# Performance work log

Hardware: AMD Instinct MI355X
Metric: run time of the kernel (lower is better)

Reference implementation:

```python
import jax, jax.numpy as jnp
import numpy as np

# Module hyper-parameters (match init_kwargs)
WIN = 64        # windowSize -> N
REC = 128       # receptiveSize -> M
H = 8           # numHeads
D = 32          # headDim
DIM = 256       # dim
MAXD = WIN + (REC - WIN) // 2  # maxDisparity = 96

# Static relative position index table, shape (N, M), values in [0, 2*MAXD)
_coords_x = np.arange(WIN)[:, None]
_coords_x_ = (np.arange(REC) - (REC - WIN) // 2)[None, :]
REL_IDX = jnp.asarray(_coords_x - _coords_x_ + MAXD, dtype=jnp.int32)


def setup_inputs() -> dict:
    key = jax.random.key(0)
    ks = jax.random.split(key, 12)
    B, nW = 4, 256
    B_ = B * nW
    x = jax.random.normal(ks[0], (B_, WIN, DIM), jnp.float32)
    x_ = jax.random.normal(ks[1], (B_, REC, DIM), jnp.float32)
    mask_left = jax.random.randint(ks[2], (2, WIN, REC), 0, 2, jnp.int32)
    mask_right = jax.random.randint(ks[3], (2, WIN, REC), 0, 2, jnp.int32)
    s = 0.02
    q_w = jax.random.normal(ks[4], (DIM, H * D), jnp.float32) * s
    q_b = jnp.zeros((H * D,), jnp.float32)
    kv_w = jax.random.normal(ks[5], (DIM, 2 * H * D), jnp.float32) * s
    kv_b = jnp.zeros((2 * H * D,), jnp.float32)
    proj_w = jax.random.normal(ks[6], (H * D, DIM), jnp.float32) * s
    proj_b = jnp.zeros((DIM,), jnp.float32)
    bias_table = jax.random.normal(ks[7], (2 * MAXD, H), jnp.float32) * s
    return dict(x=x, x_=x_, mask_left=mask_left, mask_right=mask_right, nW=nW,
                q_w=q_w, q_b=q_b, kv_w=kv_w, kv_b=kv_b,
                proj_w=proj_w, proj_b=proj_b, bias_table=bias_table)


def reference(x, x_, mask_left, mask_right, nW, q_w, q_b, kv_w, kv_b, proj_w, proj_b, bias_table):
    B_, N, C = x.shape
    M = x_.shape[1]
    B = B_ // nW
    scale = D ** -0.5

    q = (x @ q_w + q_b).reshape(B_, N, H, D).transpose(0, 2, 1, 3)   # b h n d
    kv = x_ @ kv_w + kv_b
    k, v = jnp.split(kv, 2, axis=-1)
    k = k.reshape(B_, M, H, D).transpose(0, 2, 1, 3)                 # b h m d
    v = v.reshape(B_, M, H, D).transpose(0, 2, 1, 3)                 # b h m d

    attn = jnp.einsum('bhnd,bhmd->bhnm', q, k) * scale
    # gathered relative position bias: (N, M, H) -> (H, N, M)
    bias = bias_table[REL_IDX].transpose(2, 0, 1)
    attn = attn + bias[None]

    mask_value = -jnp.finfo(attn.dtype).max
    attn = attn.reshape(B, nW, H, N, M)
    mc = min(mask_left.shape[0], nW)  # static python int
    ml = (mask_left[:mc] == 1)[None, :, None]        # (1, mc, 1, N, M)
    attn = attn.at[:, :mc].set(jnp.where(ml, mask_value, attn[:, :mc]))
    mr = (mask_right[mask_right.shape[0] - mc:] == 1)[None, :, None]
    attn = attn.at[:, nW - mc:].set(jnp.where(mr, mask_value, attn[:, nW - mc:]))
    attn = attn.reshape(B_, H, N, M)

    attn = jax.nn.softmax(attn, axis=-1)
    out = jnp.einsum('bhnm,bhmd->bhnd', attn, v)
    out = out.transpose(0, 2, 1, 3).reshape(B_, N, H * D)
    out = out @ proj_w + proj_b
    return out
```

## Files before the change

### kernel.cpp

```cpp
#include <hip/hip_runtime.h>
#include <float.h>


typedef __attribute__((ext_vector_type(8))) short bf16x8;
typedef __attribute__((ext_vector_type(4))) float f32x4;

static __device__ __forceinline__ unsigned int f2bf(float f) {
    unsigned int u = __float_as_uint(f);
    return (u + 0x7FFFu + ((u >> 16) & 1u)) >> 16;
}
static __device__ __forceinline__ unsigned int pack2(float lo, float hi) {
    return f2bf(lo) | (f2bf(hi) << 16);
}

__device__ unsigned short g_Wt[262144];

__global__ __launch_bounds__(256) void prep_wt(
    const float* __restrict__ q_w, const float* __restrict__ kv_w, const float* __restrict__ proj_w)
{
    const int gid = blockIdx.x * 256 + threadIdx.x;
    int rel, ncs; const float* src;
    if (gid < 65536)       { rel = gid;          src = q_w;    ncs = 256; }
    else if (gid < 196608) { rel = gid - 65536;  src = kv_w;   ncs = 512; }
    else                   { rel = gid - 196608; src = proj_w; ncs = 256; }
    const int tl = rel >> 11, i = rel & 2047;
    const int ct = tl >> 3,  ks = tl & 7;
    const int col = i >> 5,  si = i & 31;
    const int kl = ((2 * si) ^ ((col & 3) << 4)) >> 1;
    g_Wt[gid] = (unsigned short)f2bf(src[(ks * 32 + kl) * ncs + ct * 64 + col]);
}

template<int NC, int WT_OFF, bool ABF16, bool F32OUT>
__global__ __launch_bounds__(256) void gemm_t(
    const void* __restrict__ Ain, const float* __restrict__ bias, void* __restrict__ Cout)
{
    constexpr int NCT = NC / 64;
    __shared__ __align__(16) unsigned short As[2][4096];
    __shared__ __align__(16) unsigned short Ws[2][2048];

    const int nbx = 8 * NCT;
    const int g = blockIdx.x / nbx, r = blockIdx.x % nbx;
    const int bn = r >> 3, bm = g * 8 + (r & 7);
    const size_t r0 = (size_t)bm * 128;
    const int c0 = bn * 64;

    const int t = threadIdx.x;
    const int wave = t >> 6, lane = t & 63;
    const int lr = lane & 15, hi = lane >> 4;
    const int rw = (wave >> 1) * 64, cw = (wave & 1) * 32;

    const int arow = t >> 1, aseg = t & 1;
    const int aswz = (arow & 3) << 4;
    const int ao0 = (aseg * 32) ^ aswz, ao1 = (aseg * 32 + 16) ^ aswz;

    f32x4 acc[4][2];
    #pragma unroll
    for (int i = 0; i < 4; ++i)
        #pragma unroll
        for (int j = 0; j < 2; ++j) acc[i][j] = (f32x4){0.f, 0.f, 0.f, 0.f};

    float4 ra0, ra1, ra2, ra3;
    uint4  rb0, rb1;
    uint4  rwv;

#define GLOAD(S)                                                                           \
    {                                                                                      \
        rwv = *(const uint4*)(g_Wt + WT_OFF + ((size_t)(bn * 8 + (S)) << 11) + t * 8);     \
        if (ABF16) {                                                                       \
            const unsigned short* asrc = (const unsigned short*)Ain + (r0 + arow) * 256 + (S) * 32 + aseg * 16; \
            rb0 = *(const uint4*)asrc; rb1 = *(const uint4*)(asrc + 8);                    \
        } else {                                                                           \
            const float* asrc = (const float*)Ain + (r0 + arow) * 256 + (S) * 32 + aseg * 16; \
            ra0 = *(const float4*)asrc;       ra1 = *(const float4*)(asrc + 4);            \
            ra2 = *(const float4*)(asrc + 8); ra3 = *(const float4*)(asrc + 12);           \
        }                                                                                  \
    }

#define SWRITE(B)                                                                          \
    {                                                                                      \
        uint4 u0, u1;                                                                      \
        if (ABF16) { u0 = rb0; u1 = rb1; }                                                 \
        else {                                                                             \
            u0 = make_uint4(pack2(ra0.x, ra0.y), pack2(ra0.z, ra0.w),                      \
                            pack2(ra1.x, ra1.y), pack2(ra1.z, ra1.w));                     \
            u1 = make_uint4(pack2(ra2.x, ra2.y), pack2(ra2.z, ra2.w),                      \
                            pack2(ra3.x, ra3.y), pack2(ra3.z, ra3.w));                     \
        }                                                                                  \
        char* ad = (char*)As[B] + arow * 64;                                               \
        *(uint4*)(ad + ao0) = u0; *(uint4*)(ad + ao1) = u1;                                \
        *(uint4*)((char*)Ws[B] + t * 16) = rwv;                                            \
    }

#define COMPUTE(B)                                                                         \
    {                                                                                      \
        const char* Ab = (const char*)As[B];                                               \
        const char* Wb = (const char*)Ws[B];                                               \
        const int ko = (16 * hi) ^ ((lr & 3) << 4);                                        \
        bf16x8 af0 = *(const bf16x8*)(Ab + (rw +      lr) * 64 + ko);                      \
        bf16x8 af1 = *(const bf16x8*)(Ab + (rw + 16 + lr) * 64 + ko);                      \
        bf16x8 af2 = *(const bf16x8*)(Ab + (rw + 32 + lr) * 64 + ko);                      \
        bf16x8 af3 = *(const bf16x8*)(Ab + (rw + 48 + lr) * 64 + ko);                      \
        bf16x8 bg0 = *(const bf16x8*)(Wb + (cw +      lr) * 64 + ko);                      \
        bf16x8 bg1 = *(const bf16x8*)(Wb + (cw + 16 + lr) * 64 + ko);                      \
        acc[0][0] = __builtin_amdgcn_mfma_f32_16x16x32_bf16(af0, bg0, acc[0][0], 0, 0, 0); \
        acc[0][1] = __builtin_amdgcn_mfma_f32_16x16x32_bf16(af0, bg1, acc[0][1], 0, 0, 0); \
        acc[1][0] = __builtin_amdgcn_mfma_f32_16x16x32_bf16(af1, bg0, acc[1][0], 0, 0, 0); \
        acc[1][1] = __builtin_amdgcn_mfma_f32_16x16x32_bf16(af1, bg1, acc[1][1], 0, 0, 0); \
        acc[2][0] = __builtin_amdgcn_mfma_f32_16x16x32_bf16(af2, bg0, acc[2][0], 0, 0, 0); \
        acc[2][1] = __builtin_amdgcn_mfma_f32_16x16x32_bf16(af2, bg1, acc[2][1], 0, 0, 0); \
        acc[3][0] = __builtin_amdgcn_mfma_f32_16x16x32_bf16(af3, bg0, acc[3][0], 0, 0, 0); \
        acc[3][1] = __builtin_amdgcn_mfma_f32_16x16x32_bf16(af3, bg1, acc[3][1], 0, 0, 0); \
    }

    GLOAD(0); SWRITE(0); __syncthreads();

    #pragma unroll 8
    for (int s = 0; s < 8; ++s) {
        if (s < 7) GLOAD(s + 1);
        COMPUTE(s & 1);
        if (s < 7) {
            SWRITE((s + 1) & 1);
            __syncthreads();
        }
    }

#undef GLOAD
#undef SWRITE
#undef COMPUTE

    #pragma unroll
    for (int i = 0; i < 4; ++i) {
        #pragma unroll
        for (int bj = 0; bj < 2; ++bj) {
            const int col = c0 + cw + bj * 16 + lr;
            const float bb = bias[col];
            #pragma unroll
            for (int q = 0; q < 4; ++q) {
                const size_t row = r0 + rw + i * 16 + 4 * hi + q;
                const float val = acc[i][bj][q] + bb;
                if (F32OUT) ((float*)Cout)[row * NC + col] = val;
                else        ((unsigned short*)Cout)[row * NC + col] = (unsigned short)f2bf(val);
            }
        }
    }
}

__global__ __launch_bounds__(256) void attn_fused(
    const unsigned short* __restrict__ qbf, const unsigned short* __restrict__ kvbf,
    const float* __restrict__ bias_table, const int* __restrict__ mask_left,
    const int* __restrict__ mask_right, unsigned short* __restrict__ aout)
{
    __shared__ __align__(16) unsigned short Qn[64 * 32];
    __shared__ __align__(16) unsigned short Kn[128 * 32];
    __shared__ __align__(16) unsigned short Vt[32 * 128];
    __shared__ __align__(16) unsigned short Pn[64 * 128];
    __shared__ float ballT[8 * 192];

    const int w = blockIdx.x;
    const int t = threadIdx.x;
    const int wave = t >> 6, lane = t & 63;
    const int lr = lane & 15, hi = lane >> 4;
    const int n0w = wave * 16;

    for (int i = t; i < 1536; i += 256) {
        const int hh = i / 192, r = i - hh * 192;
        ballT[i] = bias_table[r * 8 + hh];
    }

    const int wi = w & 255;
    const int* mbase = nullptr;
    if (wi < 2) mbase = mask_left + wi * (64 * 128);
    else if (wi >= 254) mbase = mask_right + (wi - 254) * (64 * 128);

    const float scale = 0.17677669529663687f;

    for (int h = 0; h < 8; ++h) {
        __syncthreads();
        {
            const int n = t >> 2, dq = t & 3;
            const uint4 v = *(const uint4*)(qbf + ((size_t)(w * 64 + n)) * 256 + h * 32 + dq * 8);
            *(uint4*)((char*)Qn + n * 64 + dq * 16) = v;
        }
        #pragma unroll
        for (int i = 0; i < 2; ++i) {
            const int m = (t >> 2) + 64 * i, dq = t & 3;
            const uint4 v = *(const uint4*)(kvbf + ((size_t)(w * 128 + m)) * 512 + h * 32 + dq * 8);
            *(uint4*)((char*)Kn + m * 64 + dq * 16) = v;
        }
        #pragma unroll
        for (int i = 0; i < 2; ++i) {
            const int db = (t >> 7) * 2 + i, m = t & 127;
            const uint4 v = *(const uint4*)(kvbf + ((size_t)(w * 128 + m)) * 512 + 256 + h * 32 + db * 8);
            const unsigned short* vs = (const unsigned short*)&v;
            #pragma unroll
            for (int e = 0; e < 8; ++e) {
                const int d = db * 8 + e;
                *(unsigned short*)((char*)Vt + d * 256 + ((2 * m) ^ ((d & 7) << 4))) = vs[e];
            }
        }
        __syncthreads();

        const bf16x8 qa = *(const bf16x8*)((char*)Qn + (n0w + lr) * 64 + 16 * hi);
        f32x4 sacc[8];
        #pragma unroll
        for (int mj = 0; mj < 8; ++mj) {
            sacc[mj] = (f32x4){0.f, 0.f, 0.f, 0.f};
            const bf16x8 kb = *(const bf16x8*)((char*)Kn + (mj * 16 + lr) * 64 + 16 * hi);
            sacc[mj] = __builtin_amdgcn_mfma_f32_16x16x32_bf16(qa, kb, sacc[mj], 0, 0, 0);
        }

        const float* bh = ballT + h * 192;
        #pragma unroll
        for (int mj = 0; mj < 8; ++mj) {
            const int m = 16 * mj + lr;
            #pragma unroll
            for (int q = 0; q < 4; ++q) {
                const int n = n0w + 4 * hi + q;
                sacc[mj][q] = fmaf(sacc[mj][q], scale, bh[n - m + 128]);
            }
        }
        if (mbase) {
            #pragma unroll
            for (int mj = 0; mj < 8; ++mj) {
                const int m = 16 * mj + lr;
                #pragma unroll
                for (int q = 0; q < 4; ++q) {
                    const int n = n0w + 4 * hi + q;
                    if (mbase[n * 128 + m] == 1) sacc[mj][q] = -FLT_MAX;
                }
            }
        }

        float inv[4];
        #pragma unroll
        for (int q = 0; q < 4; ++q) {
            float mx = sacc[0][q];
            #pragma unroll
            for (int mj = 1; mj < 8; ++mj) mx = fmaxf(mx, sacc[mj][q]);
            mx = fmaxf(mx, __shfl_xor(mx, 1));
            mx = fmaxf(mx, __shfl_xor(mx, 2));
            mx = fmaxf(mx, __shfl_xor(mx, 4));
            mx = fmaxf(mx, __shfl_xor(mx, 8));
            float sm = 0.f;
            #pragma unroll
            for (int mj = 0; mj < 8; ++mj) {
                sacc[mj][q] = __expf(sacc[mj][q] - mx);
                sm += sacc[mj][q];
            }
            sm += __shfl_xor(sm, 1);
            sm += __shfl_xor(sm, 2);
            sm += __shfl_xor(sm, 4);
            sm += __shfl_xor(sm, 8);
            inv[q] = 1.0f / sm;
        }

        #pragma unroll
        for (int mj = 0; mj < 8; ++mj) {
            #pragma unroll
            for (int q = 0; q < 4; ++q) {
                const float pv = sacc[mj][q];
                const float po = __shfl_xor(pv, 1);
                if (!(lane & 1)) {
                    const int n = n0w + 4 * hi + q;
                    const int m = 16 * mj + lr;
                    const unsigned int u = f2bf(pv) | (f2bf(po) << 16);
                    *(unsigned int*)((char*)Pn + n * 256 + ((2 * m) ^ ((n & 7) << 4))) = u;
                }
            }
        }

        f32x4 oacc[2];
        oacc[0] = (f32x4){0.f, 0.f, 0.f, 0.f};
        oacc[1] = (f32x4){0.f, 0.f, 0.f, 0.f};
        const int nA = n0w + lr;
        const int swzA = (nA & 7) << 4;
        #pragma unroll
        for (int kk = 0; kk < 4; ++kk) {
            const bf16x8 pa = *(const bf16x8*)((char*)Pn + nA * 256 + ((64 * kk + 16 * hi) ^ swzA));
            #pragma unroll
            for (int j = 0; j < 2; ++j) {
                const int d = j * 16 + lr;
                const bf16x8 vb = *(const bf16x8*)((char*)Vt + d * 256 + ((64 * kk + 16 * hi) ^ ((d & 7) << 4)));
                oacc[j] = __builtin_amdgcn_mfma_f32_16x16x32_bf16(pa, vb, oacc[j], 0, 0, 0);
            }
        }
        #pragma unroll
        for (int j = 0; j < 2; ++j) {
            #pragma unroll
            for (int q = 0; q < 4; ++q) {
                const int n = n0w + 4 * hi + q;
                aout[((size_t)(w * 64 + n)) * 256 + h * 32 + j * 16 + lr] =
                    (unsigned short)f2bf(oacc[j][q] * inv[q]);
            }
        }
    }
}

extern "C" void kernel_launch(void* const* d_in, const int* in_sizes, int n_in,
                              void* d_out, int out_size, void* d_ws, size_t ws_size,
                              hipStream_t stream)
{
    const float* x      = (const float*)d_in[0];
    const float* x_     = (const float*)d_in[1];
    const int*   mask_l = (const int*)d_in[2];
    const int*   mask_r = (const int*)d_in[3];
    const float* q_w    = (const float*)d_in[5];
    const float* q_b    = (const float*)d_in[6];
    const float* kv_w   = (const float*)d_in[7];
    const float* kv_b   = (const float*)d_in[8];
    const float* proj_w = (const float*)d_in[9];
    const float* proj_b = (const float*)d_in[10];
    const float* bias_t = (const float*)d_in[11];

    unsigned short* qbf  = (unsigned short*)d_ws;
    unsigned short* kvbf = qbf + (size_t)65536 * 256;
    float* out = (float*)d_out;

    prep_wt<<<1024, 256, 0, stream>>>(q_w, kv_w, proj_w);
    gemm_t<256, 0,      false, false><<<2048, 256, 0, stream>>>(x,  q_b,  qbf);
    gemm_t<512, 65536,  false, false><<<8192, 256, 0, stream>>>(x_, kv_b, kvbf);
    attn_fused<<<1024, 256, 0, stream>>>(qbf, kvbf, bias_t, mask_l, mask_r, qbf);
    gemm_t<256, 196608, true,  true ><<<2048, 256, 0, stream>>>(qbf, proj_b, out);
}
```

Measured before the change: 302.2 us.

## Fuse KV projection GEMM into attention kernel, computing K/V per head in LDS

Removes the separate KV projection GEMM and its bf16 global intermediate. Each attention block now loads its 128x256 slice of x_ into LDS as bf16 and computes K and V per head with MFMA, staging the weight slice in LDS. This saves the global write and reread of the KV tensor and one kernel launch. In exchange, LDS use per block grows a lot (about 64KB for XL plus 32KB for weights), which lowers occupancy, and the weights are reloaded from global memory for each head in each block.

Measured after the change: 319.9 us. 5.9% more time.

```diff
diff --git a/kernel.cpp b/kernel.cpp
--- a/kernel.cpp
+++ b/kernel.cpp
@@ -145,26 +145,52 @@
     }
 }
 
-__global__ __launch_bounds__(256) void attn_fused(
-    const unsigned short* __restrict__ qbf, const unsigned short* __restrict__ kvbf,
-    const float* __restrict__ bias_table, const int* __restrict__ mask_left,
-    const int* __restrict__ mask_right, unsigned short* __restrict__ aout)
+__global__ __launch_bounds__(256) void attn_kv(
+    const unsigned short* __restrict__ qbf, const float* __restrict__ x_,
+    const float* __restrict__ kv_bias, const float* __restrict__ bias_table,
+    const int* __restrict__ mask_left, const int* __restrict__ mask_right,
+    unsigned short* __restrict__ aout)
 {
-    __shared__ __align__(16) unsigned short Qn[64 * 32];
+    __shared__ __align__(16) unsigned short XL[128 * 256];
+    __shared__ __align__(16) unsigned short W2s[8 * 2048];
     __shared__ __align__(16) unsigned short Kn[128 * 32];
     __shared__ __align__(16) unsigned short Vt[32 * 128];
     __shared__ __align__(16) unsigned short Pn[64 * 128];
+    __shared__ __align__(16) unsigned short Qn[64 * 32];
     __shared__ float ballT[8 * 192];
+    __shared__ float kvb[512];
 
     const int w = blockIdx.x;
     const int t = threadIdx.x;
     const int wave = t >> 6, lane = t & 63;
     const int lr = lane & 15, hi = lane >> 4;
     const int n0w = wave * 16;
+    const int rw4 = wave * 32;
 
     for (int i = t; i < 1536; i += 256) {
-        const int hh = i / 192, r = i - hh * 192;
-        ballT[i] = bias_table[r * 8 + hh];
+        const int hh = i / 192, rr = i - hh * 192;
+        ballT[i] = bias_table[rr * 8 + hh];
+    }
+    kvb[t] = kv_bias[t];
+    kvb[t + 256] = kv_bias[t + 256];
+
+    {
+        const int row = t >> 1, half = t & 1;
+        const float* src = x_ + ((size_t)(w * 128 + row)) * 256 + half * 128;
+        char* dst = (char*)XL + row * 512;
+        const int swz = (row & 7) << 4;
+        #pragma unroll 2
+        for (int u = 0; u < 8; ++u) {
+            const float4 a = *(const float4*)(src + u * 16);
+            const float4 b = *(const float4*)(src + u * 16 + 4);
+            const float4 c = *(const float4*)(src + u * 16 + 8);
+            const float4 d = *(const float4*)(src + u * 16 + 12);
+            const int base = half * 256 + u * 32;
+            *(uint4*)(dst + (base ^ swz)) =
+                make_uint4(pack2(a.x, a.y), pack2(a.z, a.w), pack2(b.x, b.y), pack2(b.z, b.w));
+            *(uint4*)(dst + ((base + 16) ^ swz)) =
+                make_uint4(pack2(c.x, c.y), pack2(c.z, c.w), pack2(d.x, d.y), pack2(d.z, d.w));
+        }
     }
 
     const int wi = w & 255;
@@ -176,26 +202,75 @@
 
     for (int h = 0; h < 8; ++h) {
         __syncthreads();
+
+        {
+            const uint4* wsrc = (const uint4*)(g_Wt + 65536);
+            uint4* wdst = (uint4*)W2s;
+            const int ctK = h >> 1, half = h & 1;
+            #pragma unroll
+            for (int u = 0; u < 8; ++u) {
+                const int idx = t + u * 256;
+                const int ks = idx >> 8;
+                const int kvh = (idx >> 7) & 1;
+                const int off = idx & 127;
+                const int ct = kvh ? (4 + ctK) : ctK;
+                wdst[idx] = wsrc[(ct * 8 + ks) * 256 + half * 128 + off];
+            }
+        }
         {
             const int n = t >> 2, dq = t & 3;
             const uint4 v = *(const uint4*)(qbf + ((size_t)(w * 64 + n)) * 256 + h * 32 + dq * 8);
             *(uint4*)((char*)Qn + n * 64 + dq * 16) = v;
         }
+        __syncthreads();
+
+        f32x4 kacc[2][4];
+        #pragma unroll
+        for (int i = 0; i < 2; ++i)
+            #pragma unroll
+            for (int j = 0; j < 4; ++j) kacc[i][j] = (f32x4){0.f, 0.f, 0.f, 0.f};
+
+        {
+            const int swzX = (lr & 7) << 4;
+            const int ko2  = (16 * hi) ^ ((lr & 3) << 4);
+            #pragma unroll
+            for (int ks = 0; ks < 8; ++ks) {
+                const int koX = (ks * 64 + 16 * hi) ^ swzX;
+                const bf16x8 af0 = *(const bf16x8*)((char*)XL + (rw4 +      lr) * 512 + koX);
+                const bf16x8 af1 = *(const bf16x8*)((char*)XL + (rw4 + 16 + lr) * 512 + koX);
+                const char* wb = (const char*)W2s + ks * 4096;
+                #pragma unroll
+                for (int j = 0; j < 4; ++j) {
+                    const bf16x8 bfr = *(const bf16x8*)(wb + (j * 16 + lr) * 64 + ko2);
+                    kacc[0][j] = __builtin_amdgcn_mfma_f32_16x16x32_bf16(af0, bfr, kacc[0][j], 0, 0, 0);
+                    kacc[1][j] = __builtin_amdgcn_mfma_f32_16x16x32_bf16(af1, bfr, kacc[1][j], 0, 0, 0);
+                }
+            }
+        }
         #pragma unroll
         for (int i = 0; i < 2; ++i) {
-            const int m = (t >> 2) + 64 * i, dq = t & 3;
-            const uint4 v = *(const uint4*)(kvbf + ((size_t)(w * 128 + m)) * 512 + h * 32 + dq * 8);
-            *(uint4*)((char*)Kn + m * 64 + dq * 16) = v;
-        }
-        #pragma unroll
-        for (int i = 0; i < 2; ++i) {
-            const int db = (t >> 7) * 2 + i, m = t & 127;
-            const uint4 v = *(const uint4*)(kvbf + ((size_t)(w * 128 + m)) * 512 + 256 + h * 32 + db * 8);
-            const unsigned short* vs = (const unsigned short*)&v;
-            #pragma unroll
-            for (int e = 0; e < 8; ++e) {
-                const int d = db * 8 + e;
-                *(unsigned short*)((char*)Vt + d * 256 + ((2 * m) ^ ((d & 7) << 4))) = vs[e];
+            #pragma unroll
+            for (int j = 0; j < 2; ++j) {
+                const int d = j * 16 + lr;
+                const float bb = kvb[h * 32 + d];
+                #pragma unroll
+                for (int q = 0; q < 4; ++q) {
+                    const float kv_ = kacc[i][j][q] + bb;
+                    const float po = __shfl_xor(kv_, 1);
+                    if (!(lane & 1)) {
+                        const int m = rw4 + i * 16 + 4 * hi + q;
+                        *(unsigned int*)((char*)Kn + m * 64 + 2 * d) = f2bf(kv_) | (f2bf(po) << 16);
+                    }
+                }
+            }
+            #pragma unroll
+            for (int j = 2; j < 4; ++j) {
+                const int d = (j - 2) * 16 + lr;
+                const float bb = kvb[256 + h * 32 + d];
+                const int m0 = rw4 + i * 16 + 4 * hi;
+                const unsigned int lo = pack2(kacc[i][j][0] + bb, kacc[i][j][1] + bb);
+                const unsigned int h2 = pack2(kacc[i][j][2] + bb, kacc[i][j][3] + bb);
+                *(uint2*)((char*)Vt + d * 256 + ((2 * m0) ^ ((d & 7) << 4))) = make_uint2(lo, h2);
             }
         }
         __syncthreads();
@@ -263,8 +338,8 @@
                 if (!(lane & 1)) {
                     const int n = n0w + 4 * hi + q;
                     const int m = 16 * mj + lr;
-                    const unsigned int u = f2bf(pv) | (f2bf(po) << 16);
-                    *(unsigned int*)((char*)Pn + n * 256 + ((2 * m) ^ ((n & 7) << 4))) = u;
+                    *(unsigned int*)((char*)Pn + n * 256 + ((2 * m) ^ ((n & 7) << 4))) =
+                        f2bf(pv) | (f2bf(po) << 16);
                 }
             }
         }
@@ -312,13 +387,11 @@
     const float* proj_b = (const float*)d_in[10];
     const float* bias_t = (const float*)d_in[11];
 
-    unsigned short* qbf  = (unsigned short*)d_ws;
-    unsigned short* kvbf = qbf + (size_t)65536 * 256;
+    unsigned short* qbf = (unsigned short*)d_ws;
     float* out = (float*)d_out;
 
     prep_wt<<<1024, 256, 0, stream>>>(q_w, kv_w, proj_w);
-    gemm_t<256, 0,      false, false><<<2048, 256, 0, stream>>>(x,  q_b,  qbf);
-    gemm_t<512, 65536,  false, false><<<8192, 256, 0, stream>>>(x_, kv_b, kvbf);
-    attn_fused<<<1024, 256, 0, stream>>>(qbf, kvbf, bias_t, mask_l, mask_r, qbf);
+    gemm_t<256, 0,      false, false><<<2048, 256, 0, stream>>>(x, q_b, qbf);
+    attn_kv<<<1024, 256, 0, stream>>>(qbf, x_, kv_b, bias_t, mask_l, mask_r, qbf);
     gemm_t<256, 196608, true,  true ><<<2048, 256, 0, stream>>>(qbf, proj_b, out);
 }
```
